# Optimization experiments

Measured on AMD Instinct MI355X. Metric: run time of the kernel, lower is better.

The kernel has to match this reference:

```python
import jax, jax.numpy as jnp
import numpy as np

D_IN = 2048
D_OUT = 2048
LN_EPS = 1e-5


def setup_inputs() -> dict:
    key = jax.random.key(0)
    kx, kw, kb = jax.random.split(key, 3)
    x = jax.random.normal(kx, (8, 2048, D_IN), dtype=jnp.float32)
    # LayerNorm affine params (torch defaults: ones / zeros)
    gamma = jnp.ones((D_IN,), dtype=jnp.float32)
    beta = jnp.zeros((D_IN,), dtype=jnp.float32)
    # weight = rand(out,in)*0.001, bias = rand(out)*0.001, alpha = ones(out)
    weight = jax.random.uniform(kw, (D_OUT, D_IN), dtype=jnp.float32) * 0.001
    bias = jax.random.uniform(kb, (D_OUT,), dtype=jnp.float32) * 0.001
    alpha = jnp.ones((D_OUT,), dtype=jnp.float32)
    return {"x": x, "gamma": gamma, "beta": beta, "weight": weight,
            "bias": bias, "alpha": alpha}


def reference(x, gamma, beta, weight, bias, alpha):
    # LayerNorm over last dim (biased variance, eps=1e-5, affine)
    mu = jnp.mean(x, axis=-1, keepdims=True)
    var = jnp.mean(jnp.square(x - mu), axis=-1, keepdims=True)
    xn = (x - mu) * jax.lax.rsqrt(var + LN_EPS) * gamma + beta
    # Binarize activations: hard sign
    a = jnp.sign(xn)
    # Binarize weights: mean-center per output row, clip, sign (STE in fwd == sign)
    centered = weight - jnp.mean(weight, axis=1, keepdims=True)  # [O, I]
    signed_w = jnp.sign(centered)
    # Linear + bias, then per-output-channel alpha scale
    out = jnp.einsum('bsi,oi->bso', a, signed_w) + bias
    return out * alpha
```

## Files before the change

### kernel.cpp

```cpp
#include <hip/hip_runtime.h>

#define DIN 2048
#define WPR 64
#define QPR 32
#define GPR 16
#define RPB 8
#define LN_EPS 1e-5f

#define GLOBAL_AS __attribute__((address_space(1)))
#define LDS_AS    __attribute__((address_space(3)))

typedef unsigned long long u64;
typedef int   i32x4  __attribute__((ext_vector_type(4)));
typedef int   i32x8  __attribute__((ext_vector_type(8)));
typedef float f32x16 __attribute__((ext_vector_type(16)));

__device__ inline float wave_sum(float v) {
    #pragma unroll
    for (int off = 32; off; off >>= 1) v += __shfl_down(v, off, 64);
    return v;
}


__global__ __launch_bounds__(256) void expand_kernel(const float* __restrict__ x,
                                                     const float* __restrict__ gamma,
                                                     const float* __restrict__ beta,
                                                     const float* __restrict__ w,
                                                     char* __restrict__ Aexp,
                                                     char* __restrict__ Bexp,
                                                     int Mblocks) {
    const int t = threadIdx.x;
    const int wid = t >> 6, lane = t & 63;
    __shared__ float red[4][2 * RPB];
    __shared__ __align__(16) unsigned stg[RPB * 256];

    const bool isA = (int)blockIdx.x < Mblocks;
    const int r0 = (isA ? (int)blockIdx.x : ((int)blockIdx.x - Mblocks)) * RPB;
    const float* src = isA ? x : w;

    float gg[8], bb[8];
    if (isA) {
        float4 g0 = ((const float4*)gamma)[t * 2];
        float4 g1 = ((const float4*)gamma)[t * 2 + 1];
        float4 b0 = ((const float4*)beta)[t * 2];
        float4 b1 = ((const float4*)beta)[t * 2 + 1];
        gg[0]=g0.x; gg[1]=g0.y; gg[2]=g0.z; gg[3]=g0.w;
        gg[4]=g1.x; gg[5]=g1.y; gg[6]=g1.z; gg[7]=g1.w;
        bb[0]=b0.x; bb[1]=b0.y; bb[2]=b0.z; bb[3]=b0.w;
        bb[4]=b1.x; bb[5]=b1.y; bb[6]=b1.z; bb[7]=b1.w;
    }

    float vv[RPB][8];
    #pragma unroll
    for (int rr = 0; rr < RPB; ++rr) {
        const float* xr = src + (size_t)(r0 + rr) * DIN;
        float4 v0 = ((const float4*)xr)[t * 2];
        float4 v1 = ((const float4*)xr)[t * 2 + 1];
        vv[rr][0]=v0.x; vv[rr][1]=v0.y; vv[rr][2]=v0.z; vv[rr][3]=v0.w;
        vv[rr][4]=v1.x; vv[rr][5]=v1.y; vv[rr][6]=v1.z; vv[rr][7]=v1.w;
    }

    #pragma unroll
    for (int rr = 0; rr < RPB; ++rr) {
        float s = 0.f, ss = 0.f;
        #pragma unroll
        for (int j = 0; j < 8; ++j) s += vv[rr][j];
        if (isA) {
            #pragma unroll
            for (int j = 0; j < 8; ++j) ss += vv[rr][j] * vv[rr][j];
        }
        s = wave_sum(s);
        if (isA) ss = wave_sum(ss);
        if (lane == 0) { red[wid][rr * 2] = s; red[wid][rr * 2 + 1] = ss; }
    }
    __syncthreads();

    #pragma unroll
    for (int rr = 0; rr < RPB; ++rr) {
        float tot = red[0][rr*2] + red[1][rr*2] + red[2][rr*2] + red[3][rr*2];
        float mu  = tot * (1.f / DIN);
        unsigned word = 0;
        if (isA) {
            float tots = red[0][rr*2+1] + red[1][rr*2+1] + red[2][rr*2+1] + red[3][rr*2+1];
            float var  = tots * (1.f / DIN) - mu * mu;
            float rs   = rsqrtf(var + LN_EPS);
            #pragma unroll
            for (int j = 0; j < 8; ++j) {
                float xn = (vv[rr][j] - mu) * rs * gg[j] + bb[j];
                word |= (xn < 0.f ? 0xAu : 0x2u) << (4 * j);
            }
        } else {
            #pragma unroll
            for (int j = 0; j < 8; ++j)
                word |= ((vv[rr][j] - mu) < 0.f ? 0xAu : 0x2u) << (4 * j);
        }
        stg[rr * 256 + (((t >> 2) ^ rr) << 2) + (t & 3)] = word;
    }
    __syncthreads();

    char* dstbase = isA ? Aexp : Bexp;
    const int bm  = r0 >> 8;
    const int rt  = (r0 >> 5) & 7;
    const int ri0 = r0 & 31;
    #pragma unroll
    for (int i2 = 0; i2 < 2; ++i2) {
        const int u  = i2 * 256 + t;
        const int sc = u >> 5;
        const int kt = (u >> 4) & 1, hb = (u >> 3) & 1, ri = u & 7;
        const int g  = sc * 4 + kt * 2 + hb;
        uint4 v = *(const uint4*)&stg[ri * 256 + ((g ^ ri) << 2)];
        const size_t doff = (((size_t)(bm * 16 + sc)) * 8 + rt) * 2048 + kt * 1024 +
                            (ri0 + ri + 32 * hb) * 16;
        *(uint4*)(dstbase + doff) = v;
    }
}

__global__ __launch_bounds__(512, 2) void fp4gemm_kernel(const char* __restrict__ Aexp,
                                                         const char* __restrict__ Bexp,
                                                         const float* __restrict__ bias,
                                                         const float* __restrict__ alpha,
                                                         float* __restrict__ out,
                                                         int ldc, int nBmX) {
    __shared__ char As[3][16384];
    __shared__ char Bs[3][16384];
    const int t = threadIdx.x;
    const int wid = t >> 6, lane = t & 63;
    const int xcd = blockIdx.x & 7;
    const int loc = blockIdx.x >> 3;
    const int bm = xcd * nBmX + (loc % nBmX);
    const int bn = loc / nBmX;
    const int wr = wid >> 2;
    const int wc = wid & 3;

    const char* gA = Aexp + (size_t)bm * 16 * 16384;
    const char* gB = Bexp + (size_t)bn * 16 * 16384;

#define STAGE(BUF, S)                                                           \
    {                                                                           \
        _Pragma("unroll")                                                       \
        for (int i2 = 0; i2 < 2; ++i2) {                                        \
            const int ch = i2 * 8 + wid;                                        \
            __builtin_amdgcn_global_load_lds(                                   \
                (const GLOBAL_AS unsigned*)(gA + (size_t)(S) * 16384 + ch * 1024 + lane * 16), \
                (LDS_AS unsigned*)(&As[BUF][ch * 1024]), 16, 0, 0);             \
            __builtin_amdgcn_global_load_lds(                                   \
                (const GLOBAL_AS unsigned*)(gB + (size_t)(S) * 16384 + ch * 1024 + lane * 16), \
                (LDS_AS unsigned*)(&Bs[BUF][ch * 1024]), 16, 0, 0);             \
        }                                                                       \
    }

    f32x16 acc[4][2];
    #pragma unroll
    for (int i = 0; i < 4; ++i)
        #pragma unroll
        for (int j = 0; j < 2; ++j)
            #pragma unroll
            for (int e = 0; e < 16; ++e) acc[i][j][e] = 0.f;

    STAGE(0, 0)
    STAGE(1, 1)
    asm volatile("s_waitcnt vmcnt(4)" ::: "memory");
    __builtin_amdgcn_s_barrier();
    asm volatile("" ::: "memory");

    int c = 0;
    #pragma unroll 1
    for (int s = 0; s < 16; ++s) {
        if (s <= 13) {
            const int nb = (c == 0) ? 2 : c - 1;
            STAGE(nb, s + 2)
        }
        #pragma unroll
        for (int kt = 0; kt < 2; ++kt) {
            i32x4 a[4], b[2];
            #pragma unroll
            for (int i = 0; i < 4; ++i)
                a[i] = *(const i32x4*)&As[c][(wr * 4 + i) * 2048 + kt * 1024 + lane * 16];
            #pragma unroll
            for (int j = 0; j < 2; ++j)
                b[j] = *(const i32x4*)&Bs[c][(wc * 2 + j) * 2048 + kt * 1024 + lane * 16];
            i32x8 aa[4], bb2[2];
            #pragma unroll
            for (int i = 0; i < 4; ++i) {
                aa[i][0]=a[i][0]; aa[i][1]=a[i][1]; aa[i][2]=a[i][2]; aa[i][3]=a[i][3];
                aa[i][4]=a[i][0]; aa[i][5]=a[i][1]; aa[i][6]=a[i][2]; aa[i][7]=a[i][3];
            }
            #pragma unroll
            for (int j = 0; j < 2; ++j) {
                bb2[j][0]=b[j][0]; bb2[j][1]=b[j][1]; bb2[j][2]=b[j][2]; bb2[j][3]=b[j][3];
                bb2[j][4]=b[j][0]; bb2[j][5]=b[j][1]; bb2[j][6]=b[j][2]; bb2[j][7]=b[j][3];
            }
            __builtin_amdgcn_s_setprio(1);
            #pragma unroll
            for (int i = 0; i < 4; ++i)
                #pragma unroll
                for (int j = 0; j < 2; ++j)
                    acc[i][j] = __builtin_amdgcn_mfma_scale_f32_32x32x64_f8f6f4(
                        aa[i], bb2[j], acc[i][j], 4, 4,
                        0, 0x7F7F7F7F, 0, 0x7F7F7F7F);
            __builtin_amdgcn_s_setprio(0);
        }
        if (s == 15) break;
        if (s <= 13) { asm volatile("s_waitcnt vmcnt(4)" ::: "memory"); }
        else         { asm volatile("s_waitcnt vmcnt(0)" ::: "memory"); }
        __builtin_amdgcn_s_barrier();
        asm volatile("" ::: "memory");
        c = (c == 2) ? 0 : c + 1;
    }
#undef STAGE

    const int cl = lane & 31;
    const int rb = 4 * (lane >> 5);
    #pragma unroll
    for (int i = 0; i < 4; ++i) {
        #pragma unroll
        for (int j = 0; j < 2; ++j) {
            const int col = bn * 256 + (wc * 2 + j) * 32 + cl;
            const float bi = bias[col], al = alpha[col];
            const int row0 = bm * 256 + (wr * 4 + i) * 32 + rb;
            #pragma unroll
            for (int reg = 0; reg < 16; ++reg) {
                const int row = row0 + (reg & 3) + 8 * (reg >> 2);
                __builtin_nontemporal_store((acc[i][j][reg] + bi) * al,
                                            &out[(size_t)row * ldc + col]);
            }
        }
    }
}

__global__ __launch_bounds__(256) void w_pack_kernel(const float* __restrict__ w,
                                                     unsigned* __restrict__ wpk) {
    const int row = blockIdx.x;
    const int t = threadIdx.x;
    const float* wr = w + (size_t)row * DIN;
    float4 v0 = ((const float4*)wr)[t * 2];
    float4 v1 = ((const float4*)wr)[t * 2 + 1];
    float s = v0.x + v0.y + v0.z + v0.w + v1.x + v1.y + v1.z + v1.w;

    __shared__ float red[4];
    float wsum = wave_sum(s);
    int wid = t >> 6, lane = t & 63;
    if (lane == 0) red[wid] = wsum;
    __syncthreads();
    float mu = (red[0] + red[1] + red[2] + red[3]) * (1.f / DIN);

    float vv[8] = {v0.x, v0.y, v0.z, v0.w, v1.x, v1.y, v1.z, v1.w};
    unsigned byte = 0;
    #pragma unroll
    for (int j = 0; j < 8; ++j)
        byte |= ((vv[j] - mu) < 0.f ? 1u : 0u) << j;

    __shared__ unsigned char bytes[256];
    bytes[t] = (unsigned char)byte;
    __syncthreads();
    if (t < 64) {
        unsigned wd = (unsigned)bytes[t * 4] | ((unsigned)bytes[t * 4 + 1] << 8) |
                      ((unsigned)bytes[t * 4 + 2] << 16) | ((unsigned)bytes[t * 4 + 3] << 24);
        wpk[(size_t)row * WPR + t] = wd;
    }
}

__global__ __launch_bounds__(256) void ln_pack_kernel(const float* __restrict__ x,
                                                      const float* __restrict__ gamma,
                                                      const float* __restrict__ beta,
                                                      unsigned* __restrict__ apk) {
    const int row = blockIdx.x;
    const int t = threadIdx.x;
    const float* xr = x + (size_t)row * DIN;
    float4 v0 = ((const float4*)xr)[t * 2];
    float4 v1 = ((const float4*)xr)[t * 2 + 1];
    float s  = v0.x + v0.y + v0.z + v0.w + v1.x + v1.y + v1.z + v1.w;
    float ss = v0.x * v0.x + v0.y * v0.y + v0.z * v0.z + v0.w * v0.w +
               v1.x * v1.x + v1.y * v1.y + v1.z * v1.z + v1.w * v1.w;

    __shared__ float red[8];
    float wsum = wave_sum(s), wssum = wave_sum(ss);
    int wid = t >> 6, lane = t & 63;
    if (lane == 0) { red[wid] = wsum; red[4 + wid] = wssum; }
    __syncthreads();
    float tot  = red[0] + red[1] + red[2] + red[3];
    float tots = red[4] + red[5] + red[6] + red[7];
    float mu  = tot * (1.f / DIN);
    float var = tots * (1.f / DIN) - mu * mu;
    float rs  = rsqrtf(var + LN_EPS);

    float4 g0 = ((const float4*)gamma)[t * 2];
    float4 g1 = ((const float4*)gamma)[t * 2 + 1];
    float4 b0 = ((const float4*)beta)[t * 2];
    float4 b1 = ((const float4*)beta)[t * 2 + 1];
    float vv[8] = {v0.x, v0.y, v0.z, v0.w, v1.x, v1.y, v1.z, v1.w};
    float gg[8] = {g0.x, g0.y, g0.z, g0.w, g1.x, g1.y, g1.z, g1.w};
    float bb[8] = {b0.x, b0.y, b0.z, b0.w, b1.x, b1.y, b1.z, b1.w};
    unsigned byte = 0;
    #pragma unroll
    for (int j = 0; j < 8; ++j) {
        float xn = (vv[j] - mu) * rs * gg[j] + bb[j];
        byte |= (xn < 0.f ? 1u : 0u) << j;
    }

    __shared__ unsigned char bytes[256];
    bytes[t] = (unsigned char)byte;
    __syncthreads();
    if (t < 64) {
        unsigned wd = (unsigned)bytes[t * 4] | ((unsigned)bytes[t * 4 + 1] << 8) |
                      ((unsigned)bytes[t * 4 + 2] << 16) | ((unsigned)bytes[t * 4 + 3] << 24);
        apk[(size_t)row * WPR + t] = wd;
    }
}

__global__ __launch_bounds__(256) void bingemm_kernel(const u64* __restrict__ A,
                                                      const u64* __restrict__ B,
                                                      const float* __restrict__ bias,
                                                      const float* __restrict__ alpha,
                                                      float* __restrict__ out) {
    __shared__ u64 S[2 * 128 * QPR];
    uint4* Sg = (uint4*)S;
    const int t = threadIdx.x;
    const int bn = blockIdx.x, bm = blockIdx.y;

    const uint4* Ag = (const uint4*)(A + (size_t)bm * 128 * QPR);
    #pragma unroll
    for (int i = 0; i < 8; ++i) {
        int id = t + i * 256;
        int row = id >> 4, g = id & 15;
        Sg[(row << 4) + (g ^ (row & 15))] = Ag[id];
    }
    const uint4* Bg = (const uint4*)(B + (size_t)bn * 128 * QPR);
    #pragma unroll
    for (int i = 0; i < 8; ++i) {
        int id = t + i * 256;
        int row = id >> 4, g = id & 15;
        Sg[2048 + (row << 4) + (g ^ (row & 15))] = Bg[id];
    }
    __syncthreads();

    const int tr = t >> 4;
    const int tc = t & 15;
    const ulonglong2* Sq = (const ulonglong2*)S;
    const int abase = tr * GPR;
    const int bbase = 2048 + tc * GPR;

    int acc[8][8] = {};
    u64 a0[8][2], b0[8][2], a1[8][2], b1[8][2];

#define LOADK(KK, AR, BR)                                            \
    {                                                                \
        const int ka = abase + ((KK) ^ tr);                          \
        const int kb = bbase + ((KK) ^ tc);                          \
        _Pragma("unroll")                                            \
        for (int r = 0; r < 8; ++r) {                                \
            ulonglong2 v = Sq[ka + r * 256];                         \
            AR[r][0] = v.x; AR[r][1] = v.y;                          \
        }                                                            \
        _Pragma("unroll")                                            \
        for (int c2 = 0; c2 < 8; ++c2) {                             \
            ulonglong2 v = Sq[kb + c2 * 256];                        \
            BR[c2][0] = v.x; BR[c2][1] = v.y;                        \
        }                                                            \
    }

#define COMPK(AR, BR)                                                \
    {                                                                \
        _Pragma("unroll")                                            \
        for (int r = 0; r < 8; ++r) {                                \
            _Pragma("unroll")                                        \
            for (int c2 = 0; c2 < 8; ++c2) {                         \
                acc[r][c2] += __popcll(AR[r][0] ^ BR[c2][0]);        \
                acc[r][c2] += __popcll(AR[r][1] ^ BR[c2][1]);        \
            }                                                        \
        }                                                            \
    }

    LOADK(0, a0, b0);
    #pragma unroll 1
    for (int kk = 0; kk < 14; kk += 2) {
        LOADK(kk + 1, a1, b1);
        COMPK(a0, b0);
        LOADK(kk + 2, a0, b0);
        COMPK(a1, b1);
    }
    LOADK(15, a1, b1);
    COMPK(a0, b0);
    COMPK(a1, b1);
#undef LOADK
#undef COMPK

    float bi[8], al[8];
    #pragma unroll
    for (int c2 = 0; c2 < 8; ++c2) {
        int col = bn * 128 + tc + 16 * c2;
        bi[c2] = bias[col];
        al[c2] = alpha[col];
    }
    #pragma unroll
    for (int r = 0; r < 8; ++r) {
        const size_t row = (size_t)bm * 128 + tr + 16 * r;
        float* op = out + row * 2048 + bn * 128 + tc;
        #pragma unroll
        for (int c2 = 0; c2 < 8; ++c2)
            op[16 * c2] = ((float)(DIN - 2 * acc[r][c2]) + bi[c2]) * al[c2];
    }
}

extern "C" void kernel_launch(void* const* d_in, const int* in_sizes, int n_in,
                              void* d_out, int out_size, void* d_ws, size_t ws_size,
                              hipStream_t stream) {
    const float* x     = (const float*)d_in[0];
    const float* gamma = (const float*)d_in[1];
    const float* beta  = (const float*)d_in[2];
    const float* w     = (const float*)d_in[3];
    const float* bias  = (const float*)d_in[4];
    const float* alpha = (const float*)d_in[5];
    float* out = (float*)d_out;

    const int M = in_sizes[0] / DIN;
    const int N = in_sizes[3] / DIN;

    const size_t needA = (size_t)M * (DIN / 2);
    const size_t needB = (size_t)N * (DIN / 2);

    if (ws_size >= needA + needB && (M % 2048) == 0 && N == 2048) {
        char* Aexp = (char*)d_ws;
        char* Bexp = (char*)d_ws + needA;
        expand_kernel<<<(M + N) / RPB, 256, 0, stream>>>(x, gamma, beta, w,
                                                         Aexp, Bexp, M / RPB);
        const int nBmX = (M / 256) / 8;
        dim3 grid((N / 256) * (M / 256));
        fp4gemm_kernel<<<grid, 512, 0, stream>>>(Aexp, Bexp, bias, alpha, out,
                                                 N, nBmX);
    } else {
        unsigned* apk = (unsigned*)d_ws;
        unsigned* wpk = (unsigned*)((char*)d_ws + (size_t)M * WPR * 4);
        w_pack_kernel<<<N, 256, 0, stream>>>(w, wpk);
        ln_pack_kernel<<<M, 256, 0, stream>>>(x, gamma, beta, apk);
        dim3 grid(N / 128, M / 128);
        bingemm_kernel<<<grid, 256, 0, stream>>>((const u64*)apk, (const u64*)wpk,
                                                 bias, alpha, out);
    }
}
```

Baseline: 85.94 us.

## Interleave global-to-LDS staging with MFMA phases in the binary GEMM main loop

Splits each K-stage into four phases, one per A row-block. Each phase issues one quarter of the next stage's global_load_lds traffic alongside its LDS reads and MFMAs. B fragments are hoisted and loaded once per stage, and barriers are added between phases. The goal is to spread memory issue across the compute so loads and MFMAs overlap better. The cost is three extra workgroup barriers per stage and explicit lgkmcnt waits, which may serialize waves.

```diff
diff --git a/kernel.cpp b/kernel.cpp
--- a/kernel.cpp
+++ b/kernel.cpp
@@ -135,14 +135,14 @@
     const char* gA = Aexp + (size_t)bm * 16 * 16384;
     const char* gB = Bexp + (size_t)bn * 16 * 16384;
 
-#define STAGE(BUF, S)                                                           \
+#define STAGE_Q(BUF, S, PH)                                                     \
     {                                                                           \
-        _Pragma("unroll")                                                       \
-        for (int i2 = 0; i2 < 2; ++i2) {                                        \
-            const int ch = i2 * 8 + wid;                                        \
+        const int ch = ((PH) >> 1) * 8 + wid;                                   \
+        if (((PH) & 1) == 0) {                                                  \
             __builtin_amdgcn_global_load_lds(                                   \
                 (const GLOBAL_AS unsigned*)(gA + (size_t)(S) * 16384 + ch * 1024 + lane * 16), \
                 (LDS_AS unsigned*)(&As[BUF][ch * 1024]), 16, 0, 0);             \
+        } else {                                                                \
             __builtin_amdgcn_global_load_lds(                                   \
                 (const GLOBAL_AS unsigned*)(gB + (size_t)(S) * 16384 + ch * 1024 + lane * 16), \
                 (LDS_AS unsigned*)(&Bs[BUF][ch * 1024]), 16, 0, 0);             \
@@ -157,8 +157,8 @@
             #pragma unroll
             for (int e = 0; e < 16; ++e) acc[i][j][e] = 0.f;
 
-    STAGE(0, 0)
-    STAGE(1, 1)
+    STAGE_Q(0, 0, 0) STAGE_Q(0, 0, 1) STAGE_Q(0, 0, 2) STAGE_Q(0, 0, 3)
+    STAGE_Q(1, 1, 0) STAGE_Q(1, 1, 1) STAGE_Q(1, 1, 2) STAGE_Q(1, 1, 3)
     asm volatile("s_waitcnt vmcnt(4)" ::: "memory");
     __builtin_amdgcn_s_barrier();
     asm volatile("" ::: "memory");
@@ -166,39 +166,44 @@
     int c = 0;
     #pragma unroll 1
     for (int s = 0; s < 16; ++s) {
-        if (s <= 13) {
-            const int nb = (c == 0) ? 2 : c - 1;
-            STAGE(nb, s + 2)
-        }
-        #pragma unroll
-        for (int kt = 0; kt < 2; ++kt) {
-            i32x4 a[4], b[2];
-            #pragma unroll
-            for (int i = 0; i < 4; ++i)
-                a[i] = *(const i32x4*)&As[c][(wr * 4 + i) * 2048 + kt * 1024 + lane * 16];
-            #pragma unroll
-            for (int j = 0; j < 2; ++j)
-                b[j] = *(const i32x4*)&Bs[c][(wc * 2 + j) * 2048 + kt * 1024 + lane * 16];
-            i32x8 aa[4], bb2[2];
-            #pragma unroll
-            for (int i = 0; i < 4; ++i) {
-                aa[i][0]=a[i][0]; aa[i][1]=a[i][1]; aa[i][2]=a[i][2]; aa[i][3]=a[i][3];
-                aa[i][4]=a[i][0]; aa[i][5]=a[i][1]; aa[i][6]=a[i][2]; aa[i][7]=a[i][3];
+        const int nb = (c == 0) ? 2 : c - 1;
+        const bool dostage = (s <= 13);
+
+        i32x8 bb2[2][2];
+        #pragma unroll
+        for (int kt = 0; kt < 2; ++kt)
+            #pragma unroll
+            for (int j = 0; j < 2; ++j) {
+                i32x4 v = *(const i32x4*)&Bs[c][(wc * 2 + j) * 2048 + kt * 1024 + lane * 16];
+                bb2[kt][j][0]=v[0]; bb2[kt][j][1]=v[1]; bb2[kt][j][2]=v[2]; bb2[kt][j][3]=v[3];
+                bb2[kt][j][4]=v[0]; bb2[kt][j][5]=v[1]; bb2[kt][j][6]=v[2]; bb2[kt][j][7]=v[3];
             }
-            #pragma unroll
-            for (int j = 0; j < 2; ++j) {
-                bb2[j][0]=b[j][0]; bb2[j][1]=b[j][1]; bb2[j][2]=b[j][2]; bb2[j][3]=b[j][3];
-                bb2[j][4]=b[j][0]; bb2[j][5]=b[j][1]; bb2[j][6]=b[j][2]; bb2[j][7]=b[j][3];
+
+        #pragma unroll
+        for (int ph = 0; ph < 4; ++ph) {
+            i32x4 a0 = *(const i32x4*)&As[c][(wr * 4 + ph) * 2048 + 0 * 1024 + lane * 16];
+            i32x4 a1 = *(const i32x4*)&As[c][(wr * 4 + ph) * 2048 + 1 * 1024 + lane * 16];
+            if (dostage) STAGE_Q(nb, s + 2, ph)
+            i32x8 aa0, aa1;
+            aa0[0]=a0[0]; aa0[1]=a0[1]; aa0[2]=a0[2]; aa0[3]=a0[3];
+            aa0[4]=a0[0]; aa0[5]=a0[1]; aa0[6]=a0[2]; aa0[7]=a0[3];
+            aa1[0]=a1[0]; aa1[1]=a1[1]; aa1[2]=a1[2]; aa1[3]=a1[3];
+            aa1[4]=a1[0]; aa1[5]=a1[1]; aa1[6]=a1[2]; aa1[7]=a1[3];
+            asm volatile("s_waitcnt lgkmcnt(0)" ::: "memory");
+            __builtin_amdgcn_s_setprio(1);
+            acc[ph][0] = __builtin_amdgcn_mfma_scale_f32_32x32x64_f8f6f4(
+                aa0, bb2[0][0], acc[ph][0], 4, 4, 0, 0x7F7F7F7F, 0, 0x7F7F7F7F);
+            acc[ph][1] = __builtin_amdgcn_mfma_scale_f32_32x32x64_f8f6f4(
+                aa0, bb2[0][1], acc[ph][1], 4, 4, 0, 0x7F7F7F7F, 0, 0x7F7F7F7F);
+            acc[ph][0] = __builtin_amdgcn_mfma_scale_f32_32x32x64_f8f6f4(
+                aa1, bb2[1][0], acc[ph][0], 4, 4, 0, 0x7F7F7F7F, 0, 0x7F7F7F7F);
+            acc[ph][1] = __builtin_amdgcn_mfma_scale_f32_32x32x64_f8f6f4(
+                aa1, bb2[1][1], acc[ph][1], 4, 4, 0, 0x7F7F7F7F, 0, 0x7F7F7F7F);
+            __builtin_amdgcn_s_setprio(0);
+            if (ph < 3) {
+                __builtin_amdgcn_s_barrier();
+                asm volatile("" ::: "memory");
             }
-            __builtin_amdgcn_s_setprio(1);
-            #pragma unroll
-            for (int i = 0; i < 4; ++i)
-                #pragma unroll
-                for (int j = 0; j < 2; ++j)
-                    acc[i][j] = __builtin_amdgcn_mfma_scale_f32_32x32x64_f8f6f4(
-                        aa[i], bb2[j], acc[i][j], 4, 4,
-                        0, 0x7F7F7F7F, 0, 0x7F7F7F7F);
-            __builtin_amdgcn_s_setprio(0);
         }
         if (s == 15) break;
         if (s <= 13) { asm volatile("s_waitcnt vmcnt(4)" ::: "memory"); }
@@ -207,7 +212,7 @@
         asm volatile("" ::: "memory");
         c = (c == 2) ? 0 : c + 1;
     }
-#undef STAGE
+#undef STAGE_Q
 
     const int cl = lane & 31;
     const int rb = 4 * (lane >> 5);
```

Measured after the change: 86.44 us. Within noise of the previous version (+0.6%).
